# Optimization experiments

Hardware: AMD Instinct MI355X
Metric: run time of the kernel (lower is better)

Reference implementation:

```python
import jax, jax.numpy as jnp
import numpy as np

B, T, D, N = 2, 2048, 1024, 16
H = D // N  # 64

def setup_inputs() -> dict:
    key = jax.random.key(0)
    ks = jax.random.split(key, 5)
    s = 0.02
    return {
        "x": jax.random.normal(ks[0], (B, T, D), dtype=jnp.float32),
        "w_attn": jax.random.normal(ks[1], (D, 3 * D), dtype=jnp.float32) * s,
        "b_attn": jax.random.normal(ks[2], (3 * D,), dtype=jnp.float32) * s,
        "w_proj": jax.random.normal(ks[3], (D, D), dtype=jnp.float32) * s,
        "b_proj": jax.random.normal(ks[4], (D,), dtype=jnp.float32) * s,
    }

def reference(x, w_attn, b_attn, w_proj, b_proj):
    # qkv projection: (B,T,3D)
    qkv = jnp.einsum('btd,de->bte', x, w_attn) + b_attn
    q, k, v = jnp.split(qkv, 3, axis=-1)
    q = q.reshape(B, T, N, H)
    k = k.reshape(B, T, N, H)
    v = v.reshape(B, T, N, H)
    scale = jnp.asarray(H ** 0.5, dtype=x.dtype)
    # scores: (B, T_q, T_kv, N) -- matches torch einsum 'btnh,bsnh->btsn'
    scores = jnp.einsum('btnh,bsnh->btsn', q, k) / scale
    # causal mask, past_len = 0 (no kv cache)
    causal = jnp.tril(jnp.ones((T, T), dtype=bool))  # (T_q, T_kv)
    scores = jnp.where(causal[None, :, :, None], scores, jnp.asarray(-jnp.inf, dtype=scores.dtype))
    weights = jax.nn.softmax(scores, axis=2)  # softmax over kv axis
    out = jnp.einsum('btsn,bsnh->btnh', weights, v).reshape(B, T, D)
    output = jnp.einsum('btd,de->bte', out, w_proj) + b_proj
    return output, k, v
```

## Files before the change

### kernel.cpp

```cpp
#include <hip/hip_runtime.h>
#include <hip/hip_bf16.h>


typedef __attribute__((ext_vector_type(8))) short bf16x8;
typedef __attribute__((ext_vector_type(4))) float f32x4;

#define MFMA16(a, b, c) __builtin_amdgcn_mfma_f32_16x16x32_bf16(a, b, c, 0, 0, 0)

static constexpr int Bb = 2, Tt = 2048, Dd = 1024, Nn = 16, Hh = 64;
static constexpr float NEG_BIG = -30000.0f;
static constexpr float QSCALE  = 0.125f;

__device__ __forceinline__ short f2bf(float f) {
    __hip_bfloat16 h = __float2bfloat16(f);
    short s; __builtin_memcpy(&s, &h, 2); return s;
}
__device__ __forceinline__ float bf2f(short s) {
    __hip_bfloat16 h; __builtin_memcpy(&h, &s, 2); return __bfloat162float(h);
}
__device__ __forceinline__ bf16x8 cvt8(const float* __restrict__ p) {
    f32x4 a = *(const f32x4*)p, b = *(const f32x4*)(p + 4);
    bf16x8 r;
    #pragma unroll
    for (int j = 0; j < 4; ++j) { r[j] = f2bf(a[j]); r[4 + j] = f2bf(b[j]); }
    return r;
}
__device__ __forceinline__ bf16x8 cvt8s(const float* __restrict__ p, float s) {
    f32x4 a = *(const f32x4*)p, b = *(const f32x4*)(p + 4);
    bf16x8 r;
    #pragma unroll
    for (int j = 0; j < 4; ++j) { r[j] = f2bf(a[j] * s); r[4 + j] = f2bf(b[j] * s); }
    return r;
}

__device__ __forceinline__ void gload16(const short* g, short* l) {
    __builtin_amdgcn_global_load_lds(
        (const __attribute__((address_space(1))) unsigned int*)g,
        (__attribute__((address_space(3))) unsigned int*)l, 16, 0, 0);
}

template<int CTRL>
__device__ __forceinline__ float dppf(float x) {
    int i; __builtin_memcpy(&i, &x, 4);
    i = __builtin_amdgcn_update_dpp(0, i, CTRL, 0xf, 0xf, true);
    float r; __builtin_memcpy(&r, &i, 4); return r;
}
__device__ __forceinline__ float rowmax16(float x) {
    x = fmaxf(x, dppf<0x128>(x)); x = fmaxf(x, dppf<0x124>(x));
    x = fmaxf(x, dppf<0x122>(x)); x = fmaxf(x, dppf<0x121>(x));
    return x;
}
__device__ __forceinline__ float rowsum16(float x) {
    x += dppf<0x128>(x); x += dppf<0x124>(x);
    x += dppf<0x122>(x); x += dppf<0x121>(x);
    return x;
}

__global__ __launch_bounds__(256) void prep(
    const float* __restrict__ x, const float* __restrict__ wa,
    const float* __restrict__ wp,
    short* __restrict__ xb, short* __restrict__ wat, short* __restrict__ wpt)
{
    const int bid = blockIdx.x, tid = threadIdx.x;
    if (bid < 1024) {
        __shared__ float s[64][65];
        const float* src; short* dst; int Nc, k0, n0;
        if (bid < 768) { src = wa; dst = wat; Nc = 3072; k0 = (bid & 15) * 64; n0 = (bid >> 4) * 64; }
        else { int b2 = bid - 768; src = wp; dst = wpt; Nc = 1024; k0 = (b2 & 15) * 64; n0 = (b2 >> 4) * 64; }
        const int row = tid >> 2, cg = (tid & 3) * 16;
        const float* p = src + (size_t)(k0 + row) * Nc + n0 + cg;
        #pragma unroll
        for (int i = 0; i < 4; ++i) {
            f32x4 v = *(const f32x4*)(p + 4 * i);
            #pragma unroll
            for (int j = 0; j < 4; ++j) s[row][cg + 4 * i + j] = v[j];
        }
        __syncthreads();
        bf16x8 o0, o1;
        #pragma unroll
        for (int j = 0; j < 8; ++j) { o0[j] = f2bf(s[cg + j][row]); o1[j] = f2bf(s[cg + 8 + j][row]); }
        short* q = dst + (size_t)(n0 + row) * 1024 + k0 + cg;
        *(bf16x8*)q = o0; *(bf16x8*)(q + 8) = o1;
    } else {
        const size_t base = (size_t)(bid - 1024) * 2048 + tid * 8;
        *(bf16x8*)(xb + base) = cvt8(x + base);
    }
}

template<int MODE>
__global__ __launch_bounds__(MODE == 1 ? 512 : 256, MODE == 1 ? 6 : 2) void gemm128(
    const short* __restrict__ A, const short* __restrict__ Bt,
    const float* __restrict__ bias,
    float* __restrict__ fk, float* __restrict__ fv,
    short* __restrict__ qb, short* __restrict__ kb, short* __restrict__ vt,
    float* __restrict__ fout, int K)
{
    constexpr int BN = (MODE == 1) ? 128 : 64;
    __shared__ short sA[3][128][32];
    __shared__ short sB[3][BN][32];
    const int tid = threadIdx.x, lane = tid & 63, wave = tid >> 6;
    const int l15 = lane & 15, quad = lane >> 4;

    const int lid = (int)blockIdx.y * (int)gridDim.x + (int)blockIdx.x;
    const int xcd = lid & 7, sidx = lid >> 3;
    constexpr int SN = (MODE == 1) ? 12 : 8;
    const int mt = (xcd & 3) * 8 + (sidx & 7);
    const int ntl = (xcd >> 2) * SN + (sidx >> 3);
    const int m0 = mt * 128, n0 = ntl * BN;

    const int wr = (MODE == 1) ? (wave >> 2) * 64 : (wave >> 1) * 64;
    const int wc = (MODE == 1) ? (wave & 3) * 32  : (wave & 1) * 32;

    const int rl  = lane >> 2;
    const int csh = (lane & 3) * 8;
    const size_t aOff0 = (size_t)(m0 + wave * 16 + rl) * K + csh;
    const size_t aOff1 = aOff0 + (size_t)64 * K;
    const size_t bOff0 = (size_t)(n0 + wave * 16 + rl) * K + csh;

    f32x4 acc[4][2] = {};

#define STAGE_G(pp, kk)                                                \
    do {                                                               \
        gload16(A  + aOff0 + (kk), &sA[pp][wave * 16][0]);             \
        if constexpr (MODE == 2)                                       \
            gload16(A + aOff1 + (kk), &sA[pp][64 + wave * 16][0]);     \
        gload16(Bt + bOff0 + (kk), &sB[pp][wave * 16][0]);             \
    } while (0)

    STAGE_G(0, 0);
    STAGE_G(1, 32);

    int cur = 0;
    for (int k0 = 0; k0 < K; k0 += 32) {
        if (k0 + 32 < K) {
            if constexpr (MODE == 1) asm volatile("s_waitcnt vmcnt(2)" ::: "memory");
            else                     asm volatile("s_waitcnt vmcnt(3)" ::: "memory");
        } else {
            asm volatile("s_waitcnt vmcnt(0)" ::: "memory");
        }
        __builtin_amdgcn_s_barrier();
        __builtin_amdgcn_sched_barrier(0);

        const int nxt2 = cur >= 1 ? cur - 1 : cur + 2;
        if (k0 + 64 < K) STAGE_G(nxt2, k0 + 64);

        bf16x8 af[4], bfr[2];
        #pragma unroll
        for (int mt2 = 0; mt2 < 4; ++mt2) af[mt2]  = *(const bf16x8*)&sA[cur][wr + mt2 * 16 + l15][quad * 8];
        #pragma unroll
        for (int nt2 = 0; nt2 < 2; ++nt2) bfr[nt2] = *(const bf16x8*)&sB[cur][wc + nt2 * 16 + l15][quad * 8];
        #pragma unroll
        for (int mt2 = 0; mt2 < 4; ++mt2)
        #pragma unroll
        for (int nt2 = 0; nt2 < 2; ++nt2)
            acc[mt2][nt2] = MFMA16(af[mt2], bfr[nt2], acc[mt2][nt2]);

        cur = cur < 2 ? cur + 1 : 0;
    }
#undef STAGE_G

    #pragma unroll
    for (int mt2 = 0; mt2 < 4; ++mt2)
    #pragma unroll
    for (int nt2 = 0; nt2 < 2; ++nt2) {
        const int gc = n0 + wc + nt2 * 16 + l15;
        const float bv = bias[gc];
        #pragma unroll
        for (int r = 0; r < 4; ++r) {
            const int grow = m0 + wr + mt2 * 16 + quad * 4 + r;
            const float val = acc[mt2][nt2][r] + bv;
            if (MODE == 1) {
                const int reg = gc >> 10, c = gc & 1023;
                if (reg == 0) {
                    qb[(size_t)grow * 1024 + c] = f2bf(val * QSCALE);
                } else {
                    const int bidx = grow >> 11, tt = grow & 2047;
                    const int nh = c >> 6, h = c & 63;
                    if (reg == 1) {
                        fk[(size_t)grow * 1024 + c] = val;
                        kb[((size_t)(bidx * Nn + nh) * Tt + tt) * Hh + h] = f2bf(val);
                    } else {
                        fv[(size_t)grow * 1024 + c] = val;
                        vt[((size_t)(bidx * Nn + nh) * Hh + h) * Tt + tt] = f2bf(val);
                    }
                }
            } else {
                fout[(size_t)grow * 1024 + gc] = val;
            }
        }
    }
}

__global__ __launch_bounds__(512, 6) void attn5(
    const short* __restrict__ Qb, const short* __restrict__ Kb,
    const short* __restrict__ Vt,
    short* __restrict__ op_part, float* __restrict__ ls_part)
{
    const int by = 15 - (int)blockIdx.y;
    const int c  = blockIdx.z;
    if (c && by < 8) return;

    __shared__ short sK[2][64][64];
    __shared__ short sV[2][64][64];
    __shared__ short sP[8][16][72];

    const int tid = threadIdx.x, lane = tid & 63, wave = tid >> 6;
    const int l15 = lane & 15, quad = lane >> 4;
    const int head = blockIdx.x;
    const int b = head >> 4, n = head & 15;
    const int q0w = by * 128 + wave * 16;

    const int gmask = (q0w + 15) >> 6;
    const int g0 = c * 16;
    const int ntmax = min(16, 2 * by + 2 - g0);

    const size_t kvhead = (size_t)head * Tt * Hh;
    const short* kbh = Kb + kvhead;
    const short* vth = Vt + kvhead;

    const short* qp = Qb + ((size_t)b * Tt + q0w + l15) * Dd + n * Hh + quad * 8;
    const bf16x8 qf0 = *(const bf16x8*)qp;
    const bf16x8 qf1 = *(const bf16x8*)(qp + 32);

    const int sr   = wave * 8 + (lane >> 3);
    const int srcb = (((lane & 7) ^ (lane >> 3))) * 8;
    const int swz  = l15 & 7;
    const int bsw  = quad ^ swz;

    f32x4 o_acc[4] = {};
    float lsum[4] = {};

#define STAGE_KV(bb, ktb)                                               \
    do {                                                                \
        gload16(kbh + (size_t)((ktb) + sr) * Hh + srcb, &sK[bb][wave * 8][0]); \
        gload16(vth + (size_t)sr * Tt + (ktb) + srcb,   &sV[bb][wave * 8][0]); \
    } while (0)

    STAGE_KV(0, g0 * 64);
    __syncthreads();

    int buf = 0;
    for (int it = 0; it < ntmax; ++it) {
        const int kt = (g0 + it) * 64;
        if (it + 1 < ntmax) STAGE_KV(buf ^ 1, kt + 64);

        f32x4 s[4] = {};
        #pragma unroll
        for (int jp = 0; jp < 2; ++jp) {
            bf16x8 ka0 = *(const bf16x8*)&sK[buf][32 * jp      + l15][bsw * 8];
            bf16x8 kc0 = *(const bf16x8*)&sK[buf][32 * jp      + l15][(bsw ^ 4) * 8];
            bf16x8 ka1 = *(const bf16x8*)&sK[buf][32 * jp + 16 + l15][bsw * 8];
            bf16x8 kc1 = *(const bf16x8*)&sK[buf][32 * jp + 16 + l15][(bsw ^ 4) * 8];
            __builtin_amdgcn_s_setprio(1);
            s[2 * jp]     = MFMA16(qf0, ka0, s[2 * jp]);
            s[2 * jp]     = MFMA16(qf1, kc0, s[2 * jp]);
            s[2 * jp + 1] = MFMA16(qf0, ka1, s[2 * jp + 1]);
            s[2 * jp + 1] = MFMA16(qf1, kc1, s[2 * jp + 1]);
            __builtin_amdgcn_s_setprio(0);
        }

        const bool masked = (g0 + it >= gmask);
        #pragma unroll
        for (int r = 0; r < 4; ++r) {
            const int row = q0w + quad * 4 + r;
            float x0 = s[0][r], x1 = s[1][r], x2 = s[2][r], x3 = s[3][r];
            if (masked) {
                if (kt + l15      > row) x0 = NEG_BIG;
                if (kt + 16 + l15 > row) x1 = NEG_BIG;
                if (kt + 32 + l15 > row) x2 = NEG_BIG;
                if (kt + 48 + l15 > row) x3 = NEG_BIG;
            }
            const float p0 = __expf(x0), p1 = __expf(x1);
            const float p2 = __expf(x2), p3 = __expf(x3);
            lsum[r] += (p0 + p1) + (p2 + p3);
            short* pw = &sP[wave][quad * 4 + r][l15];
            pw[0] = f2bf(p0); pw[16] = f2bf(p1); pw[32] = f2bf(p2); pw[48] = f2bf(p3);
        }
        __asm__ volatile("s_waitcnt lgkmcnt(0)" ::: "memory");
        bf16x8 pf0 = *(const bf16x8*)&sP[wave][l15][quad * 8];
        bf16x8 pf1 = *(const bf16x8*)&sP[wave][l15][32 + quad * 8];
        #pragma unroll
        for (int hc = 0; hc < 4; ++hc) {
            bf16x8 v0 = *(const bf16x8*)&sV[buf][hc * 16 + l15][bsw * 8];
            bf16x8 v1 = *(const bf16x8*)&sV[buf][hc * 16 + l15][(bsw ^ 4) * 8];
            __builtin_amdgcn_s_setprio(1);
            o_acc[hc] = MFMA16(pf0, v0, o_acc[hc]);
            o_acc[hc] = MFMA16(pf1, v1, o_acc[hc]);
            __builtin_amdgcn_s_setprio(0);
        }
        __syncthreads();
        buf ^= 1;
    }
#undef STAGE_KV

    const int slot = head * 24 + (by < 8 ? by : 2 * by - 8 + c);
    short* opw = op_part + ((size_t)slot * 128 + wave * 16) * 64;
    #pragma unroll
    for (int r = 0; r < 4; ++r) {
        const float l = rowsum16(lsum[r]);
        const int rloc = quad * 4 + r;
        if (l15 == 0) ls_part[slot * 128 + wave * 16 + rloc] = l;
        #pragma unroll
        for (int hc = 0; hc < 4; ++hc)
            opw[rloc * 64 + hc * 16 + l15] = f2bf(o_acc[hc][r]);
    }
}

__global__ __launch_bounds__(256) void attn_reduce(
    const short* __restrict__ op_part, const float* __restrict__ ls_part,
    short* __restrict__ Ob)
{
    const int idx = blockIdx.x * 256 + threadIdx.x;
    const int r = idx >> 3;
    const int h0 = (idx & 7) * 8;
    const int head = r >> 11, t = r & 2047;
    const int by = t >> 7, tr = t & 127;
    const int nch = 1 + (by >= 8);
    const int base = head * 24 + (by < 8 ? by : 2 * by - 8);

    float acc[8] = {};
    float l = 0.f;
    for (int c = 0; c < nch; ++c) {
        const int slot = base + c;
        bf16x8 v = *(const bf16x8*)(op_part + ((size_t)slot * 128 + tr) * 64 + h0);
        #pragma unroll
        for (int j = 0; j < 8; ++j) acc[j] += bf2f(v[j]);
        l += ls_part[slot * 128 + tr];
    }
    const float rl = 1.0f / fmaxf(l, 1e-20f);
    bf16x8 o;
    #pragma unroll
    for (int j = 0; j < 8; ++j) o[j] = f2bf(acc[j] * rl);
    const int b = head >> 4, n = head & 15;
    *(bf16x8*)(Ob + ((size_t)(b * Tt + t)) * Dd + n * Hh + h0) = o;
}

__global__ __launch_bounds__(256) void gemm_bias_split(
    const float* __restrict__ A, const float* __restrict__ Bm,
    const float* __restrict__ bias,
    float* __restrict__ dst0, float* __restrict__ dst1, float* __restrict__ dst2,
    short* __restrict__ kb, short* __restrict__ vt,
    int K, int Ncols, int Dsplit)
{
    __shared__ short sA[64][40];
    __shared__ short sBt[64][40];
    const int tid  = threadIdx.x;
    const int lane = tid & 63;
    const int wave = tid >> 6;
    const int l15  = lane & 15;
    const int quad = lane >> 4;
    const int m0 = blockIdx.x * 64;
    const int n0 = blockIdx.y * 64;
    const int wm = (wave >> 1) * 32;
    const int wn = (wave & 1) * 32;
    const int ar = tid >> 2, ac = (tid & 3) * 8;
    const int bk = tid >> 3, bc = (tid & 7) * 8;

    f32x4 acc[2][2] = {};
    for (int k0 = 0; k0 < K; k0 += 32) {
        bf16x8 av = cvt8(A  + (size_t)(m0 + ar) * K     + k0 + ac);
        bf16x8 bv = cvt8(Bm + (size_t)(k0 + bk) * Ncols + n0 + bc);
        *(bf16x8*)&sA[ar][ac] = av;
        #pragma unroll
        for (int j = 0; j < 8; ++j) sBt[bc + j][bk] = bv[j];
        __syncthreads();
        bf16x8 a0 = *(const bf16x8*)&sA[wm + l15][quad * 8];
        bf16x8 a1 = *(const bf16x8*)&sA[wm + 16 + l15][quad * 8];
        bf16x8 b0 = *(const bf16x8*)&sBt[wn + l15][quad * 8];
        bf16x8 b1 = *(const bf16x8*)&sBt[wn + 16 + l15][quad * 8];
        acc[0][0] = MFMA16(a0, b0, acc[0][0]);
        acc[0][1] = MFMA16(a0, b1, acc[0][1]);
        acc[1][0] = MFMA16(a1, b0, acc[1][0]);
        acc[1][1] = MFMA16(a1, b1, acc[1][1]);
        __syncthreads();
    }
    #pragma unroll
    for (int i = 0; i < 2; ++i)
    #pragma unroll
    for (int j = 0; j < 2; ++j) {
        const int ncol = n0 + wn + j * 16 + l15;
        const float bvf = bias[ncol];
        float* dbase; int c, which;
        if (ncol < Dsplit)        { dbase = dst0; c = ncol;            which = 0; }
        else if (ncol < 2*Dsplit) { dbase = dst1; c = ncol - Dsplit;   which = 1; }
        else                      { dbase = dst2; c = ncol - 2*Dsplit; which = 2; }
        const int nh = c >> 6, h = c & 63;
        #pragma unroll
        for (int r = 0; r < 4; ++r) {
            const int mrow = m0 + wm + i * 16 + quad * 4 + r;
            const float val = acc[i][j][r] + bvf;
            dbase[(size_t)mrow * Dsplit + c] = val;
            if (which == 1 && kb) {
                const int bidx = mrow >> 11, tt = mrow & 2047;
                kb[((size_t)(bidx * Nn + nh) * Tt + tt) * Hh + h] = f2bf(val);
            } else if (which == 2 && vt) {
                const int bidx = mrow >> 11, tt = mrow & 2047;
                vt[((size_t)(bidx * Nn + nh) * Hh + h) * Tt + tt] = f2bf(val);
            }
        }
    }
}

__global__ __launch_bounds__(256) void attn_fast(
    const float* __restrict__ Q, const short* __restrict__ Kb,
    const short* __restrict__ Vt, float* __restrict__ O)
{
    __shared__ short sP[4][2][16][40];
    const int tid  = threadIdx.x;
    const int lane = tid & 63;
    const int wave = tid >> 6;
    const int l15  = lane & 15;
    const int quad = lane >> 4;
    const int b = blockIdx.x >> 4, n = blockIdx.x & 15;
    const int qg = ((int)gridDim.y - 1 - (int)blockIdx.y) * 4 + wave;
    const int q0 = qg * 16;

    const size_t ohead  = (size_t)b * Tt * Dd + (size_t)n * Hh;
    const size_t kvhead = (size_t)(b * Nn + n) * Tt * Hh;
    const short* kbh = Kb + kvhead;
    const short* vth = Vt + kvhead;

    const float* qrow = Q + ohead + (size_t)(q0 + l15) * Dd;
    const bf16x8 qf0 = cvt8s(qrow + quad * 8, QSCALE);
    const bf16x8 qf1 = cvt8s(qrow + 32 + quad * 8, QSCALE);

    float m_i[4], l_i[4];
    f32x4 o_acc[4] = {};
    #pragma unroll
    for (int r = 0; r < 4; ++r) { m_i[r] = NEG_BIG; l_i[r] = 0.f; }

    int par = 0;
    for (int kt = 0; kt < q0 + 16; kt += 32, par ^= 1) {
        f32x4 s0 = {}, s1 = {};
        {
            const short* k0 = kbh + (size_t)(kt + l15) * Hh + quad * 8;
            bf16x8 k0a = *(const bf16x8*)k0;
            bf16x8 k0b = *(const bf16x8*)(k0 + 32);
            const short* k1 = k0 + 16 * Hh;
            bf16x8 k1a = *(const bf16x8*)k1;
            bf16x8 k1b = *(const bf16x8*)(k1 + 32);
            s0 = MFMA16(qf0, k0a, s0); s0 = MFMA16(qf1, k0b, s0);
            s1 = MFMA16(qf0, k1a, s1); s1 = MFMA16(qf1, k1b, s1);
        }
        const int qr0 = q0 + quad * 4;
        #pragma unroll
        for (int r = 0; r < 4; ++r) {
            float x0 = (kt + l15      > qr0 + r) ? NEG_BIG : s0[r];
            float x1 = (kt + 16 + l15 > qr0 + r) ? NEG_BIG : s1[r];
            const float t  = rowmax16(fmaxf(x0, x1));
            const float mn = fmaxf(m_i[r], t);
            const float alpha = __expf(m_i[r] - mn);
            const float p0 = __expf(x0 - mn);
            const float p1 = __expf(x1 - mn);
            l_i[r] = l_i[r] * alpha + rowsum16(p0 + p1);
            m_i[r] = mn;
            #pragma unroll
            for (int hc = 0; hc < 4; ++hc) o_acc[hc][r] *= alpha;
            sP[wave][par][quad * 4 + r][l15]      = f2bf(p0);
            sP[wave][par][quad * 4 + r][16 + l15] = f2bf(p1);
        }
        __asm__ volatile("s_waitcnt lgkmcnt(0)" ::: "memory");
        bf16x8 pf = *(const bf16x8*)&sP[wave][par][l15][quad * 8];
        #pragma unroll
        for (int hc = 0; hc < 4; ++hc) {
            bf16x8 vf = *(const bf16x8*)(vth + (size_t)(hc * 16 + l15) * Tt + kt + quad * 8);
            o_acc[hc] = MFMA16(pf, vf, o_acc[hc]);
        }
    }
    #pragma unroll
    for (int r = 0; r < 4; ++r) {
        const float rl = 1.0f / fmaxf(l_i[r], 1e-20f);
        #pragma unroll
        for (int hc = 0; hc < 4; ++hc)
            O[ohead + (size_t)(q0 + quad * 4 + r) * Dd + hc * 16 + l15] = o_acc[hc][r] * rl;
    }
}

extern "C" void kernel_launch(void* const* d_in, const int* in_sizes, int n_in,
                              void* d_out, int out_size, void* d_ws, size_t ws_size,
                              hipStream_t stream) {
    const float* x      = (const float*)d_in[0];
    const float* w_attn = (const float*)d_in[1];
    const float* b_attn = (const float*)d_in[2];
    const float* w_proj = (const float*)d_in[3];
    const float* b_proj = (const float*)d_in[4];

    const size_t elems = (size_t)Bb * Tt * Dd;
    float* out  = (float*)d_out;
    float* kout = out  + elems;
    float* vout = kout + elems;

    const size_t NSLOT = (size_t)32 * 24;
    const size_t need_v2 = (4 * elems + (size_t)1024 * 1024 + NSLOT * 128 * 64) * 2
                         + NSLOT * 128 * 4;

    if (ws_size >= need_v2) {
        short* qb  = (short*)d_ws;
        short* kb  = qb + elems;
        short* vt  = kb + elems;
        short* wpt = vt + elems;
        short* xb  = wpt + (size_t)1024 * 1024;
        short* ob  = xb;
        short* op_part = xb + elems;
        float* ls_part = (float*)(op_part + NSLOT * 128 * 64);
        short* wat = op_part;

        prep<<<3072, 256, 0, stream>>>(x, w_attn, w_proj, xb, wat, wpt);
        gemm128<1><<<dim3(32, 24), 512, 0, stream>>>(
            xb, wat, b_attn, kout, vout, qb, kb, vt, nullptr, Dd);
        attn5<<<dim3(Bb * Nn, 16, 2), 512, 0, stream>>>(qb, kb, vt, op_part, ls_part);
        attn_reduce<<<2048, 256, 0, stream>>>(op_part, ls_part, ob);
        gemm128<2><<<dim3(32, 16), 256, 0, stream>>>(
            ob, wpt, b_proj, nullptr, nullptr, nullptr, nullptr, nullptr, out, Dd);
    } else {
        float* o_ws = (float*)d_ws;
        short* kb = (short*)((char*)d_ws + elems * 4);
        short* vt = kb + elems;
        gemm_bias_split<<<dim3((Bb * Tt) / 64, (3 * Dd) / 64), 256, 0, stream>>>(
            x, w_attn, b_attn, out, kout, vout, kb, vt, Dd, 3 * Dd, Dd);
        attn_fast<<<dim3(Bb * Nn, Tt / 64), 256, 0, stream>>>(out, kb, vt, o_ws);
        gemm_bias_split<<<dim3((Bb * Tt) / 64, Dd / 64), 256, 0, stream>>>(
            o_ws, w_proj, b_proj, out, out, out, nullptr, nullptr, Dd, Dd, Dd);
    }
}
```

Before: 199.4 us.

## Write unsplit attention rows directly and shrink output-projection GEMM tiles

Attention blocks for the first half of query rows, which have only one KV chunk, now normalize and write their output straight into the projection input instead of going through partial buffers. The reduce kernel therefore only handles the second-half rows that were split into two chunks, and is launched with half the grid. The output-projection GEMM moves from 128x64 to 64x64 tiles with a remapped XCD swizzle and a higher occupancy hint, doubling the block count to fill the CUs better. The cost is more total global loads of the B operand in the projection GEMM.

Measured after the change: 197.2 us (median of 2 runs). No clear change (-1.1%).

```diff
diff --git a/kernel.cpp b/kernel.cpp
--- a/kernel.cpp
+++ b/kernel.cpp
@@ -88,42 +88,41 @@
 }
 
 template<int MODE>
-__global__ __launch_bounds__(MODE == 1 ? 512 : 256, MODE == 1 ? 6 : 2) void gemm128(
+__global__ __launch_bounds__(MODE == 1 ? 512 : 256, MODE == 1 ? 6 : 4) void gemm128(
     const short* __restrict__ A, const short* __restrict__ Bt,
     const float* __restrict__ bias,
     float* __restrict__ fk, float* __restrict__ fv,
     short* __restrict__ qb, short* __restrict__ kb, short* __restrict__ vt,
     float* __restrict__ fout, int K)
 {
+    constexpr int BM = (MODE == 1) ? 128 : 64;
     constexpr int BN = (MODE == 1) ? 128 : 64;
-    __shared__ short sA[3][128][32];
+    constexpr int MF = (MODE == 1) ? 4 : 2;
+    __shared__ short sA[3][BM][32];
     __shared__ short sB[3][BN][32];
     const int tid = threadIdx.x, lane = tid & 63, wave = tid >> 6;
     const int l15 = lane & 15, quad = lane >> 4;
 
     const int lid = (int)blockIdx.y * (int)gridDim.x + (int)blockIdx.x;
     const int xcd = lid & 7, sidx = lid >> 3;
-    constexpr int SN = (MODE == 1) ? 12 : 8;
-    const int mt = (xcd & 3) * 8 + (sidx & 7);
-    const int ntl = (xcd >> 2) * SN + (sidx >> 3);
-    const int m0 = mt * 128, n0 = ntl * BN;
-
-    const int wr = (MODE == 1) ? (wave >> 2) * 64 : (wave >> 1) * 64;
+    int mt, ntl;
+    if constexpr (MODE == 1) { mt = (xcd & 3) * 8  + (sidx & 7);  ntl = (xcd >> 2) * 12 + (sidx >> 3); }
+    else                     { mt = (xcd & 3) * 16 + (sidx & 15); ntl = (xcd >> 2) * 8  + (sidx >> 4); }
+    const int m0 = mt * BM, n0 = ntl * BN;
+
+    const int wr = (MODE == 1) ? (wave >> 2) * 64 : (wave >> 1) * 32;
     const int wc = (MODE == 1) ? (wave & 3) * 32  : (wave & 1) * 32;
 
     const int rl  = lane >> 2;
     const int csh = (lane & 3) * 8;
     const size_t aOff0 = (size_t)(m0 + wave * 16 + rl) * K + csh;
-    const size_t aOff1 = aOff0 + (size_t)64 * K;
     const size_t bOff0 = (size_t)(n0 + wave * 16 + rl) * K + csh;
 
-    f32x4 acc[4][2] = {};
+    f32x4 acc[MF][2] = {};
 
 #define STAGE_G(pp, kk)                                                \
     do {                                                               \
         gload16(A  + aOff0 + (kk), &sA[pp][wave * 16][0]);             \
-        if constexpr (MODE == 2)                                       \
-            gload16(A + aOff1 + (kk), &sA[pp][64 + wave * 16][0]);     \
         gload16(Bt + bOff0 + (kk), &sB[pp][wave * 16][0]);             \
     } while (0)
 
@@ -133,8 +132,7 @@
     int cur = 0;
     for (int k0 = 0; k0 < K; k0 += 32) {
         if (k0 + 32 < K) {
-            if constexpr (MODE == 1) asm volatile("s_waitcnt vmcnt(2)" ::: "memory");
-            else                     asm volatile("s_waitcnt vmcnt(3)" ::: "memory");
+            asm volatile("s_waitcnt vmcnt(2)" ::: "memory");
         } else {
             asm volatile("s_waitcnt vmcnt(0)" ::: "memory");
         }
@@ -144,13 +142,13 @@
         const int nxt2 = cur >= 1 ? cur - 1 : cur + 2;
         if (k0 + 64 < K) STAGE_G(nxt2, k0 + 64);
 
-        bf16x8 af[4], bfr[2];
-        #pragma unroll
-        for (int mt2 = 0; mt2 < 4; ++mt2) af[mt2]  = *(const bf16x8*)&sA[cur][wr + mt2 * 16 + l15][quad * 8];
-        #pragma unroll
-        for (int nt2 = 0; nt2 < 2; ++nt2) bfr[nt2] = *(const bf16x8*)&sB[cur][wc + nt2 * 16 + l15][quad * 8];
-        #pragma unroll
-        for (int mt2 = 0; mt2 < 4; ++mt2)
+        bf16x8 af[MF], bfr[2];
+        #pragma unroll
+        for (int mt2 = 0; mt2 < MF; ++mt2) af[mt2]  = *(const bf16x8*)&sA[cur][wr + mt2 * 16 + l15][quad * 8];
+        #pragma unroll
+        for (int nt2 = 0; nt2 < 2; ++nt2)  bfr[nt2] = *(const bf16x8*)&sB[cur][wc + nt2 * 16 + l15][quad * 8];
+        #pragma unroll
+        for (int mt2 = 0; mt2 < MF; ++mt2)
         #pragma unroll
         for (int nt2 = 0; nt2 < 2; ++nt2)
             acc[mt2][nt2] = MFMA16(af[mt2], bfr[nt2], acc[mt2][nt2]);
@@ -160,7 +158,7 @@
 #undef STAGE_G
 
     #pragma unroll
-    for (int mt2 = 0; mt2 < 4; ++mt2)
+    for (int mt2 = 0; mt2 < MF; ++mt2)
     #pragma unroll
     for (int nt2 = 0; nt2 < 2; ++nt2) {
         const int gc = n0 + wc + nt2 * 16 + l15;
@@ -194,7 +192,8 @@
 __global__ __launch_bounds__(512, 6) void attn5(
     const short* __restrict__ Qb, const short* __restrict__ Kb,
     const short* __restrict__ Vt,
-    short* __restrict__ op_part, float* __restrict__ ls_part)
+    short* __restrict__ op_part, float* __restrict__ ls_part,
+    short* __restrict__ Ob)
 {
     const int by = 15 - (int)blockIdx.y;
     const int c  = blockIdx.z;
@@ -293,16 +292,28 @@
     }
 #undef STAGE_KV
 
-    const int slot = head * 24 + (by < 8 ? by : 2 * by - 8 + c);
-    short* opw = op_part + ((size_t)slot * 128 + wave * 16) * 64;
-    #pragma unroll
-    for (int r = 0; r < 4; ++r) {
-        const float l = rowsum16(lsum[r]);
-        const int rloc = quad * 4 + r;
-        if (l15 == 0) ls_part[slot * 128 + wave * 16 + rloc] = l;
-        #pragma unroll
-        for (int hc = 0; hc < 4; ++hc)
-            opw[rloc * 64 + hc * 16 + l15] = f2bf(o_acc[hc][r]);
+    if (by < 8) {
+        short* obw = Ob + ((size_t)b * Tt + q0w) * Dd + n * Hh;
+        #pragma unroll
+        for (int r = 0; r < 4; ++r) {
+            const float rlv = 1.0f / fmaxf(rowsum16(lsum[r]), 1e-20f);
+            const int rloc = quad * 4 + r;
+            #pragma unroll
+            for (int hc = 0; hc < 4; ++hc)
+                obw[(size_t)rloc * Dd + hc * 16 + l15] = f2bf(o_acc[hc][r] * rlv);
+        }
+    } else {
+        const int slot = head * 24 + 2 * by - 8 + c;
+        short* opw = op_part + ((size_t)slot * 128 + wave * 16) * 64;
+        #pragma unroll
+        for (int r = 0; r < 4; ++r) {
+            const float l = rowsum16(lsum[r]);
+            const int rloc = quad * 4 + r;
+            if (l15 == 0) ls_part[slot * 128 + wave * 16 + rloc] = l;
+            #pragma unroll
+            for (int hc = 0; hc < 4; ++hc)
+                opw[rloc * 64 + hc * 16 + l15] = f2bf(o_acc[hc][r]);
+        }
     }
 }
 
@@ -313,14 +324,14 @@
     const int idx = blockIdx.x * 256 + threadIdx.x;
     const int r = idx >> 3;
     const int h0 = (idx & 7) * 8;
-    const int head = r >> 11, t = r & 2047;
+    const int head = r >> 10, t = 1024 + (r & 1023);
     const int by = t >> 7, tr = t & 127;
-    const int nch = 1 + (by >= 8);
-    const int base = head * 24 + (by < 8 ? by : 2 * by - 8);
+    const int base = head * 24 + 2 * by - 8;
 
     float acc[8] = {};
     float l = 0.f;
-    for (int c = 0; c < nch; ++c) {
+    #pragma unroll
+    for (int c = 0; c < 2; ++c) {
         const int slot = base + c;
         bf16x8 v = *(const bf16x8*)(op_part + ((size_t)slot * 128 + tr) * 64 + h0);
         #pragma unroll
@@ -508,9 +519,9 @@
         prep<<<3072, 256, 0, stream>>>(x, w_attn, w_proj, xb, wat, wpt);
         gemm128<1><<<dim3(32, 24), 512, 0, stream>>>(
             xb, wat, b_attn, kout, vout, qb, kb, vt, nullptr, Dd);
-        attn5<<<dim3(Bb * Nn, 16, 2), 512, 0, stream>>>(qb, kb, vt, op_part, ls_part);
-        attn_reduce<<<2048, 256, 0, stream>>>(op_part, ls_part, ob);
-        gemm128<2><<<dim3(32, 16), 256, 0, stream>>>(
+        attn5<<<dim3(Bb * Nn, 16, 2), 512, 0, stream>>>(qb, kb, vt, op_part, ls_part, ob);
+        attn_reduce<<<1024, 256, 0, stream>>>(op_part, ls_part, ob);
+        gemm128<2><<<dim3(64, 16), 256, 0, stream>>>(
             ob, wpt, b_proj, nullptr, nullptr, nullptr, nullptr, nullptr, out, Dd);
     } else {
         float* o_ws = (float*)d_ws;
```
